# Kernel optimization log

Measured on AMD Instinct MI355X. Metric: run time of the kernel, lower is better.

The kernel has to match this reference:

```python
import jax, jax.numpy as jnp
import numpy as np

N = 50000   # nodes
E = 800000  # edges (avg degree 16)
F = 128     # node_features


def setup_inputs() -> dict:
    key = jax.random.key(0)
    ks = jax.random.split(key, 10)
    s = 1.0 / np.sqrt(F)
    x = jax.random.normal(ks[0], (N, F), jnp.float32)
    edge_index = jax.random.randint(ks[1], (2, E), 0, N, dtype=jnp.int32)
    edge_weight = jax.random.uniform(ks[2], (E,), jnp.float32)
    # EvolveGCNO initial weight (glorot-ish) and GRU parameters (PyTorch layout)
    W0 = jax.random.uniform(ks[3], (F, F), jnp.float32, -s, s)
    W_ih = jax.random.uniform(ks[4], (3 * F, F), jnp.float32, -s, s)
    W_hh = jax.random.uniform(ks[5], (3 * F, F), jnp.float32, -s, s)
    b_ih = jax.random.uniform(ks[6], (3 * F,), jnp.float32, -s, s)
    b_hh = jax.random.uniform(ks[7], (3 * F,), jnp.float32, -s, s)
    # Linear(F, 1) head
    w_lin = jax.random.uniform(ks[8], (1, F), jnp.float32, -s, s)
    b_lin = jax.random.uniform(ks[9], (1,), jnp.float32, -s, s)
    return dict(x=x, edge_index=edge_index, edge_weight=edge_weight, W0=W0,
                W_ih=W_ih, W_hh=W_hh, b_ih=b_ih, b_hh=b_hh,
                w_lin=w_lin, b_lin=b_lin)


def _gru_evolve(W0, W_ih, W_hh, b_ih, b_hh):
    # GRU(input=W0, hidden=W0): seq_len=1, batch=F, feature=F (PyTorch gate order r,z,n)
    gi = W0 @ W_ih.T + b_ih  # [F, 3F]
    gh = W0 @ W_hh.T + b_hh  # [F, 3F]
    f = W0.shape[1]
    i_r, i_z, i_n = gi[:, :f], gi[:, f:2 * f], gi[:, 2 * f:]
    h_r, h_z, h_n = gh[:, :f], gh[:, f:2 * f], gh[:, 2 * f:]
    r = jax.nn.sigmoid(i_r + h_r)
    z = jax.nn.sigmoid(i_z + h_z)
    n = jnp.tanh(i_n + r * h_n)
    return (1.0 - z) * n + z * W0  # evolved weight [F, F]


def reference(x, edge_index, edge_weight, W0, W_ih, W_hh, b_ih, b_hh, w_lin, b_lin):
    n_nodes = x.shape[0]
    W = _gru_evolve(W0, W_ih, W_hh, b_ih, b_hh)
    # gcn_norm: add self loops (weight 1), symmetric D^-1/2 A D^-1/2
    loop = jnp.arange(n_nodes, dtype=edge_index.dtype)
    src = jnp.concatenate([edge_index[0], loop])
    dst = jnp.concatenate([edge_index[1], loop])
    w = jnp.concatenate([edge_weight, jnp.ones((n_nodes,), x.dtype)])
    deg = jax.ops.segment_sum(w, dst, num_segments=n_nodes)
    dinv = jnp.where(deg > 0, jax.lax.rsqrt(deg), 0.0)
    norm = dinv[src] * w * dinv[dst]  # [E+N]
    xw = x @ W  # [N, F]
    h = jax.ops.segment_sum(norm[:, None] * xw[src], dst, num_segments=n_nodes)
    h = jnp.tanh(h)
    return h @ w_lin.T + b_lin  # [N, 1]
```

## Files before the change

### kernel.cpp

```cpp
#include <hip/hip_runtime.h>
#include <hip/hip_bf16.h>
#include <math.h>

#define N_NODES 50000
#define N_EDGES 800000
#define FDIM 128
#define SCAN_BLOCKS 196
#define XW_BLOCKS 391

typedef unsigned int uint32;
typedef __attribute__((ext_vector_type(8))) __bf16 bf16x8;
typedef __attribute__((ext_vector_type(8))) short short8;
typedef __attribute__((ext_vector_type(16))) float f32x16;

#define FLAG_A 200
#define FLAG_B 201
#define SCANNED 256

__device__ inline unsigned short f2bf(float f) {
  unsigned int u = __float_as_uint(f);
  unsigned int r = u + 0x7fffu + ((u >> 16) & 1u);
  return (unsigned short)(r >> 16);
}

__global__ __launch_bounds__(384) void evolve_kernel(
    const float* __restrict__ W0, const float* __restrict__ Wih,
    const float* __restrict__ Whh, const float* __restrict__ bih,
    const float* __restrict__ bhh, float* __restrict__ W,
    int* __restrict__ cnt, int* __restrict__ part) {
  int i = blockIdx.x;
  int jj = threadIdx.x;
  int gid = i * 384 + jj;
  for (int j = gid; j < N_NODES; j += 128 * 384) cnt[j] = 0;
  if (gid == 0) part[FLAG_A] = 0;
  if (gid == 1) part[FLAG_B] = 0;

  __shared__ float w0s[FDIM];
  __shared__ float gis[3 * FDIM];
  __shared__ float ghs[3 * FDIM];
  if (jj < FDIM) w0s[jj] = W0[i * FDIM + jj];
  __syncthreads();
  float gi = bih[jj], gh = bhh[jj];
  const float4* wih4 = (const float4*)(Wih + jj * FDIM);
  const float4* whh4 = (const float4*)(Whh + jj * FDIM);
#pragma unroll 8
  for (int k = 0; k < FDIM / 4; k++) {
    float4 a = wih4[k];
    float4 b = whh4[k];
    float w0a = w0s[4 * k], w0b = w0s[4 * k + 1];
    float w0c = w0s[4 * k + 2], w0d = w0s[4 * k + 3];
    gi += a.x * w0a + a.y * w0b + a.z * w0c + a.w * w0d;
    gh += b.x * w0a + b.y * w0b + b.z * w0c + b.w * w0d;
  }
  gis[jj] = gi;
  ghs[jj] = gh;
  __syncthreads();
  if (jj < FDIM) {
    float r = 1.0f / (1.0f + expf(-(gis[jj] + ghs[jj])));
    float z = 1.0f / (1.0f + expf(-(gis[jj + FDIM] + ghs[jj + FDIM])));
    float nn = tanhf(gis[jj + 2 * FDIM] + r * ghs[jj + 2 * FDIM]);
    W[i * FDIM + jj] = (1.0f - z) * nn + z * w0s[jj];
  }
}

__global__ __launch_bounds__(256) void histxw_kernel(
    const int* __restrict__ ei, int* __restrict__ cnt, int* __restrict__ rank,
    const float* __restrict__ x, const float* __restrict__ W,
    unsigned short* __restrict__ y, int n) {
  __shared__ short Bs[16 * 128 * 8];
  int t = threadIdx.x;
  if (blockIdx.x >= XW_BLOCKS) {
    int idx = (blockIdx.x - XW_BLOCKS) * 256 + t;
    if (idx < N_EDGES) {
      int dst = ei[N_EDGES + idx];
      rank[idx] = atomicAdd(&cnt[dst], 1);
    }
    return;
  }
#pragma unroll
  for (int i = 0; i < 64; i++) {
    int idx = i * 256 + t;
    int k = idx >> 7, nn = idx & 127;
    Bs[(((k >> 3) << 7) + nn) * 8 + (k & 7)] = (short)f2bf(W[idx]);
  }
  __syncthreads();

  int lane = t & 63;
  int wid = blockIdx.x * 4 + (t >> 6);
  int tr = wid * 32;
  if (tr >= n) return;
  int m = lane & 31;
  int q2 = lane >> 5;

  int row = tr + m;
  if (row >= n) row = n - 1;
  const float* xr = x + (size_t)row * FDIM;

  bf16x8 a[8];
#pragma unroll
  for (int kc = 0; kc < 8; kc++) {
    int k0 = kc * 16 + q2 * 8;
    float4 p = *(const float4*)(xr + k0);
    float4 q = *(const float4*)(xr + k0 + 4);
    short8 s;
    s[0] = (short)f2bf(p.x); s[1] = (short)f2bf(p.y);
    s[2] = (short)f2bf(p.z); s[3] = (short)f2bf(p.w);
    s[4] = (short)f2bf(q.x); s[5] = (short)f2bf(q.y);
    s[6] = (short)f2bf(q.z); s[7] = (short)f2bf(q.w);
    a[kc] = __builtin_bit_cast(bf16x8, s);
  }

  f32x16 acc[4];
#pragma unroll
  for (int ct = 0; ct < 4; ct++) {
#pragma unroll
    for (int r = 0; r < 16; r++) acc[ct][r] = 0.0f;
  }
#pragma unroll
  for (int ct = 0; ct < 4; ct++) {
    int nn = ct * 32 + m;
#pragma unroll
    for (int kc = 0; kc < 8; kc++) {
      int kg = kc * 2 + q2;
      bf16x8 b = __builtin_bit_cast(
          bf16x8, *(const short8*)(Bs + (((kg << 7) + nn) << 3)));
      acc[ct] = __builtin_amdgcn_mfma_f32_32x32x16_bf16(a[kc], b, acc[ct], 0,
                                                        0, 0);
    }
  }

#pragma unroll
  for (int r = 0; r < 16; r++) {
    int rl = (r & 3) + ((r >> 2) << 3) + (q2 << 2);
    int rg = tr + rl;
    if (rg < n) {
#pragma unroll
      for (int ct = 0; ct < 4; ct++) {
        y[(size_t)rg * FDIM + ct * 32 + m] = f2bf(acc[ct][r]);
      }
    }
  }
}

__global__ __launch_bounds__(256) void scan_all_kernel(
    const int* __restrict__ cnt, int* __restrict__ part, int* __restrict__ offs,
    int n) {
  __shared__ int tmp[256];
  int t = threadIdx.x;
  int bid = blockIdx.x;
  int idx = bid * 256 + t;
  int v = (idx < n) ? cnt[idx] : 0;
  tmp[t] = v;
  __syncthreads();
#pragma unroll
  for (int off = 1; off < 256; off <<= 1) {
    int u = (t >= off) ? tmp[t - off] : 0;
    __syncthreads();
    tmp[t] += u;
    __syncthreads();
  }
  int local_excl = tmp[t] - v;
  int block_sum = tmp[255];
  if (t == 0) {
    __hip_atomic_store(&part[bid], block_sum, __ATOMIC_RELEASE,
                       __HIP_MEMORY_SCOPE_AGENT);
    __hip_atomic_fetch_add(&part[FLAG_A], 1, __ATOMIC_ACQ_REL,
                           __HIP_MEMORY_SCOPE_AGENT);
  }
  if (bid == 0) {
    if (t == 0) {
      while (__hip_atomic_load(&part[FLAG_A], __ATOMIC_ACQUIRE,
                               __HIP_MEMORY_SCOPE_AGENT) < SCAN_BLOCKS) {
        __builtin_amdgcn_s_sleep(1);
      }
    }
    __syncthreads();
    __shared__ int ps[256];
    int pv = (t < SCAN_BLOCKS)
                 ? __hip_atomic_load(&part[t], __ATOMIC_RELAXED,
                                     __HIP_MEMORY_SCOPE_AGENT)
                 : 0;
    ps[t] = pv;
    __syncthreads();
#pragma unroll
    for (int off = 1; off < 256; off <<= 1) {
      int u = (t >= off) ? ps[t - off] : 0;
      __syncthreads();
      ps[t] += u;
      __syncthreads();
    }
    if (t < SCAN_BLOCKS)
      __hip_atomic_store(&part[SCANNED + t], ps[t] - pv, __ATOMIC_RELAXED,
                         __HIP_MEMORY_SCOPE_AGENT);
    __syncthreads();
    if (t == 0)
      __hip_atomic_store(&part[FLAG_B], 1, __ATOMIC_RELEASE,
                         __HIP_MEMORY_SCOPE_AGENT);
  }
  if (t == 0) {
    while (__hip_atomic_load(&part[FLAG_B], __ATOMIC_ACQUIRE,
                             __HIP_MEMORY_SCOPE_AGENT) == 0) {
      __builtin_amdgcn_s_sleep(1);
    }
  }
  __syncthreads();
  int base = __hip_atomic_load(&part[SCANNED + bid], __ATOMIC_RELAXED,
                               __HIP_MEMORY_SCOPE_AGENT);
  int excl = base + local_excl;
  if (idx < n) offs[idx] = excl;
  if (idx == n - 1) offs[n] = excl + v;
}

__global__ void scatter_kernel(const int* __restrict__ ei,
                               const float* __restrict__ ew,
                               const int* __restrict__ offs,
                               const int* __restrict__ rank,
                               int2* __restrict__ csr, int e) {
  int idx = blockIdx.x * blockDim.x + threadIdx.x;
  if (idx < e) {
    int src = ei[idx];
    int dst = ei[N_EDGES + idx];
    int pos = offs[dst] + rank[idx];
    csr[pos] = make_int2(src, __float_as_int(ew[idx]));
  }
}

__global__ __launch_bounds__(256) void deg_dinv_kernel(
    const int2* __restrict__ csr, const int* __restrict__ offs,
    float* __restrict__ dinv, int n) {
  int i = blockIdx.x * blockDim.x + threadIdx.x;
  if (i >= n) return;
  int b = offs[i], e = offs[i + 1];
  float d = 1.0f;
  for (int j = b; j < e; j++) d += __int_as_float(csr[j].y);
  dinv[i] = (d > 0.0f) ? rsqrtf(d) : 0.0f;
}

__global__ __launch_bounds__(256) void gather_kernel(
    const uint32* __restrict__ yb, const int* __restrict__ offs,
    const int2* __restrict__ csr, const float* __restrict__ dinv,
    const float* __restrict__ wl, const float* __restrict__ bl,
    float* __restrict__ out, int n) {
  int wid = (int)((blockIdx.x * (size_t)blockDim.x + threadIdx.x) >> 6);
  int lane = threadIdx.x & 63;
  if (wid >= n) return;
  float di = dinv[wid];
  uint32 uv = yb[(size_t)wid * 64 + lane];
  float ax = di * __uint_as_float(uv << 16);
  float ay = di * __uint_as_float(uv & 0xffff0000u);
  int beg = offs[wid], end = offs[wid + 1];
  int e = beg;
  for (; e + 4 <= end; e += 4) {
    int2 c0 = csr[e];
    int2 c1 = csr[e + 1];
    int2 c2 = csr[e + 2];
    int2 c3 = csr[e + 3];
    uint32 u0 = yb[(size_t)c0.x * 64 + lane];
    uint32 u1 = yb[(size_t)c1.x * 64 + lane];
    uint32 u2 = yb[(size_t)c2.x * 64 + lane];
    uint32 u3 = yb[(size_t)c3.x * 64 + lane];
    float w0 = __int_as_float(c0.y) * dinv[c0.x];
    float w1 = __int_as_float(c1.y) * dinv[c1.x];
    float w2 = __int_as_float(c2.y) * dinv[c2.x];
    float w3 = __int_as_float(c3.y) * dinv[c3.x];
    ax += w0 * __uint_as_float(u0 << 16);
    ay += w0 * __uint_as_float(u0 & 0xffff0000u);
    ax += w1 * __uint_as_float(u1 << 16);
    ay += w1 * __uint_as_float(u1 & 0xffff0000u);
    ax += w2 * __uint_as_float(u2 << 16);
    ay += w2 * __uint_as_float(u2 & 0xffff0000u);
    ax += w3 * __uint_as_float(u3 << 16);
    ay += w3 * __uint_as_float(u3 & 0xffff0000u);
  }
  for (; e < end; e++) {
    int2 c = csr[e];
    uint32 u = yb[(size_t)c.x * 64 + lane];
    float wn = __int_as_float(c.y) * dinv[c.x];
    ax += wn * __uint_as_float(u << 16);
    ay += wn * __uint_as_float(u & 0xffff0000u);
  }
  float2 wv = ((const float2*)wl)[lane];
  float p = tanhf(di * ax) * wv.x + tanhf(di * ay) * wv.y;
#pragma unroll
  for (int o = 32; o > 0; o >>= 1) p += __shfl_down(p, o, 64);
  if (lane == 0) out[wid] = p + bl[0];
}

extern "C" void kernel_launch(void* const* d_in, const int* in_sizes, int n_in,
                              void* d_out, int out_size, void* d_ws,
                              size_t ws_size, hipStream_t stream) {
  const float* x = (const float*)d_in[0];
  const int* ei = (const int*)d_in[1];
  const float* ew = (const float*)d_in[2];
  const float* W0 = (const float*)d_in[3];
  const float* Wih = (const float*)d_in[4];
  const float* Whh = (const float*)d_in[5];
  const float* bih = (const float*)d_in[6];
  const float* bhh = (const float*)d_in[7];
  const float* wl = (const float*)d_in[8];
  const float* bl = (const float*)d_in[9];
  float* out = (float*)d_out;

  float* ws = (float*)d_ws;
  float* W_ev = ws;
  unsigned short* y = (unsigned short*)(W_ev + 16384);
  float* dinv = (float*)(y + (size_t)N_NODES * FDIM);
  int* cnt = (int*)(dinv + N_NODES);
  int* rank = cnt + N_NODES;
  int* offs = rank + N_EDGES;
  int2* csr = (int2*)(offs + 50004);
  int* part = (int*)(csr + N_EDGES);

  evolve_kernel<<<FDIM, 384, 0, stream>>>(W0, Wih, Whh, bih, bhh, W_ev, cnt,
                                          part);
  histxw_kernel<<<XW_BLOCKS + (N_EDGES + 255) / 256, 256, 0, stream>>>(
      ei, cnt, rank, x, W_ev, y, N_NODES);
  scan_all_kernel<<<SCAN_BLOCKS, 256, 0, stream>>>(cnt, part, offs, N_NODES);
  scatter_kernel<<<(N_EDGES + 255) / 256, 256, 0, stream>>>(ei, ew, offs, rank,
                                                            csr, N_EDGES);
  deg_dinv_kernel<<<(N_NODES + 255) / 256, 256, 0, stream>>>(csr, offs, dinv,
                                                             N_NODES);
  gather_kernel<<<(N_NODES * 64) / 256, 256, 0, stream>>>(
      (const uint32*)y, offs, csr, dinv, wl, bl, out, N_NODES);
}
```

Baseline: 212.3 us.

## Fuse pipeline into two persistent kernels with grid barriers and prenormalized CSR weights

Merges the GRU evolve step into the histogram/XW kernel, with an atomic spin-wait gating the matmul blocks, and replaces the scan, scatter and degree kernels with one 196-block kernel that uses software grid barriers. It also precomputes the full symmetric normalization into the CSR weights, so the gather no longer loads dinv per edge, and unrolls the gather loop 8-wide. The aim is to cut launch overhead and the random dinv lookups in the gather. The risks are spin-wait stalls, or deadlock if not all blocks are co-resident, plus an extra serial pass over the CSR data.

Result: slower. 296.4 us (+39.6%).

```diff
diff --git a/kernel.cpp b/kernel.cpp
--- a/kernel.cpp
+++ b/kernel.cpp
@@ -5,17 +5,19 @@
 #define N_NODES 50000
 #define N_EDGES 800000
 #define FDIM 128
-#define SCAN_BLOCKS 196
+#define D2_BLOCKS 196
 #define XW_BLOCKS 391
+#define HIST_BLOCKS 3125
 
 typedef unsigned int uint32;
 typedef __attribute__((ext_vector_type(8))) __bf16 bf16x8;
 typedef __attribute__((ext_vector_type(8))) short short8;
 typedef __attribute__((ext_vector_type(16))) float f32x16;
 
-#define FLAG_A 200
-#define FLAG_B 201
-#define SCANNED 256
+#define EVOLVE_DONE 0
+#define BAR0 1
+#define SUMS 8
+#define SCANNED 208
 
 __device__ inline unsigned short f2bf(float f) {
   unsigned int u = __float_as_uint(f);
@@ -23,60 +25,71 @@
   return (unsigned short)(r >> 16);
 }
 
-__global__ __launch_bounds__(384) void evolve_kernel(
+__global__ __launch_bounds__(256) void mega1_kernel(
     const float* __restrict__ W0, const float* __restrict__ Wih,
     const float* __restrict__ Whh, const float* __restrict__ bih,
     const float* __restrict__ bhh, float* __restrict__ W,
-    int* __restrict__ cnt, int* __restrict__ part) {
-  int i = blockIdx.x;
-  int jj = threadIdx.x;
-  int gid = i * 384 + jj;
-  for (int j = gid; j < N_NODES; j += 128 * 384) cnt[j] = 0;
-  if (gid == 0) part[FLAG_A] = 0;
-  if (gid == 1) part[FLAG_B] = 0;
-
-  __shared__ float w0s[FDIM];
-  __shared__ float gis[3 * FDIM];
-  __shared__ float ghs[3 * FDIM];
-  if (jj < FDIM) w0s[jj] = W0[i * FDIM + jj];
-  __syncthreads();
-  float gi = bih[jj], gh = bhh[jj];
-  const float4* wih4 = (const float4*)(Wih + jj * FDIM);
-  const float4* whh4 = (const float4*)(Whh + jj * FDIM);
-#pragma unroll 8
-  for (int k = 0; k < FDIM / 4; k++) {
-    float4 a = wih4[k];
-    float4 b = whh4[k];
-    float w0a = w0s[4 * k], w0b = w0s[4 * k + 1];
-    float w0c = w0s[4 * k + 2], w0d = w0s[4 * k + 3];
-    gi += a.x * w0a + a.y * w0b + a.z * w0c + a.w * w0d;
-    gh += b.x * w0a + b.y * w0b + b.z * w0c + b.w * w0d;
-  }
-  gis[jj] = gi;
-  ghs[jj] = gh;
-  __syncthreads();
-  if (jj < FDIM) {
-    float r = 1.0f / (1.0f + expf(-(gis[jj] + ghs[jj])));
-    float z = 1.0f / (1.0f + expf(-(gis[jj + FDIM] + ghs[jj + FDIM])));
-    float nn = tanhf(gis[jj + 2 * FDIM] + r * ghs[jj + 2 * FDIM]);
-    W[i * FDIM + jj] = (1.0f - z) * nn + z * w0s[jj];
-  }
-}
-
-__global__ __launch_bounds__(256) void histxw_kernel(
     const int* __restrict__ ei, int* __restrict__ cnt, int* __restrict__ rank,
-    const float* __restrict__ x, const float* __restrict__ W,
-    unsigned short* __restrict__ y, int n) {
-  __shared__ short Bs[16 * 128 * 8];
+    const float* __restrict__ x, unsigned short* __restrict__ y,
+    int* __restrict__ sync, int n) {
+  __shared__ __align__(16) char smem[32768];
   int t = threadIdx.x;
-  if (blockIdx.x >= XW_BLOCKS) {
-    int idx = (blockIdx.x - XW_BLOCKS) * 256 + t;
+  int bid = blockIdx.x;
+
+  if (bid >= XW_BLOCKS) {
+    int idx = (bid - XW_BLOCKS) * 256 + t;
     if (idx < N_EDGES) {
       int dst = ei[N_EDGES + idx];
       rank[idx] = atomicAdd(&cnt[dst], 1);
     }
     return;
   }
+
+  if (bid < FDIM) {
+    float* w0s = (float*)smem;
+    float* gis = w0s + FDIM;
+    float* ghs = gis + 3 * FDIM;
+    if (t < FDIM) w0s[t] = W0[bid * FDIM + t];
+    __syncthreads();
+    for (int jj = t; jj < 3 * FDIM; jj += 256) {
+      float gi = bih[jj], gh = bhh[jj];
+      const float4* wih4 = (const float4*)(Wih + jj * FDIM);
+      const float4* whh4 = (const float4*)(Whh + jj * FDIM);
+#pragma unroll 8
+      for (int k = 0; k < FDIM / 4; k++) {
+        float4 a = wih4[k];
+        float4 b = whh4[k];
+        float w0a = w0s[4 * k], w0b = w0s[4 * k + 1];
+        float w0c = w0s[4 * k + 2], w0d = w0s[4 * k + 3];
+        gi += a.x * w0a + a.y * w0b + a.z * w0c + a.w * w0d;
+        gh += b.x * w0a + b.y * w0b + b.z * w0c + b.w * w0d;
+      }
+      gis[jj] = gi;
+      ghs[jj] = gh;
+    }
+    __syncthreads();
+    if (t < FDIM) {
+      float r = 1.0f / (1.0f + expf(-(gis[t] + ghs[t])));
+      float z = 1.0f / (1.0f + expf(-(gis[t + FDIM] + ghs[t + FDIM])));
+      float nn = tanhf(gis[t + 2 * FDIM] + r * ghs[t + 2 * FDIM]);
+      W[bid * FDIM + t] = (1.0f - z) * nn + z * w0s[t];
+      __threadfence();
+    }
+    __syncthreads();
+    if (t == 0)
+      __hip_atomic_fetch_add(&sync[EVOLVE_DONE], 1, __ATOMIC_ACQ_REL,
+                             __HIP_MEMORY_SCOPE_AGENT);
+  }
+
+  if (t == 0) {
+    while (__hip_atomic_load(&sync[EVOLVE_DONE], __ATOMIC_ACQUIRE,
+                             __HIP_MEMORY_SCOPE_AGENT) < FDIM) {
+      __builtin_amdgcn_s_sleep(2);
+    }
+  }
+  __syncthreads();
+
+  short* Bs = (short*)smem;
 #pragma unroll
   for (int i = 0; i < 64; i++) {
     int idx = i * 256 + t;
@@ -86,7 +99,7 @@
   __syncthreads();
 
   int lane = t & 63;
-  int wid = blockIdx.x * 4 + (t >> 6);
+  int wid = bid * 4 + (t >> 6);
   int tr = wid * 32;
   if (tr >= n) return;
   int m = lane & 31;
@@ -142,13 +155,28 @@
   }
 }
 
-__global__ __launch_bounds__(256) void scan_all_kernel(
-    const int* __restrict__ cnt, int* __restrict__ part, int* __restrict__ offs,
-    int n) {
+__device__ inline void grid_bar(int* ctr, int t) {
+  __syncthreads();
+  if (t == 0) {
+    __hip_atomic_fetch_add(ctr, 1, __ATOMIC_ACQ_REL, __HIP_MEMORY_SCOPE_AGENT);
+    while (__hip_atomic_load(ctr, __ATOMIC_ACQUIRE,
+                             __HIP_MEMORY_SCOPE_AGENT) < D2_BLOCKS) {
+      __builtin_amdgcn_s_sleep(1);
+    }
+  }
+  __syncthreads();
+}
+
+__global__ __launch_bounds__(256) void mega2_kernel(
+    const int* __restrict__ ei, const float* __restrict__ ew,
+    const int* __restrict__ cnt, const int* __restrict__ rank,
+    int* __restrict__ sync, int* __restrict__ lexcl, int* __restrict__ offs,
+    int2* csr, float* __restrict__ dinv, int n) {
   __shared__ int tmp[256];
-  int t = threadIdx.x;
-  int bid = blockIdx.x;
+  int t = threadIdx.x, bid = blockIdx.x;
+  const int STRIDE = D2_BLOCKS * 256;
   int idx = bid * 256 + t;
+
   int v = (idx < n) ? cnt[idx] : 0;
   tmp[t] = v;
   __syncthreads();
@@ -159,81 +187,52 @@
     tmp[t] += u;
     __syncthreads();
   }
-  int local_excl = tmp[t] - v;
-  int block_sum = tmp[255];
-  if (t == 0) {
-    __hip_atomic_store(&part[bid], block_sum, __ATOMIC_RELEASE,
-                       __HIP_MEMORY_SCOPE_AGENT);
-    __hip_atomic_fetch_add(&part[FLAG_A], 1, __ATOMIC_ACQ_REL,
-                           __HIP_MEMORY_SCOPE_AGENT);
-  }
+  if (idx < n) lexcl[idx] = tmp[t] - v;
+  if (t == 255) sync[SUMS + bid] = tmp[255];
+  grid_bar(&sync[BAR0 + 0], t);
+
   if (bid == 0) {
-    if (t == 0) {
-      while (__hip_atomic_load(&part[FLAG_A], __ATOMIC_ACQUIRE,
-                               __HIP_MEMORY_SCOPE_AGENT) < SCAN_BLOCKS) {
-        __builtin_amdgcn_s_sleep(1);
-      }
-    }
-    __syncthreads();
-    __shared__ int ps[256];
-    int pv = (t < SCAN_BLOCKS)
-                 ? __hip_atomic_load(&part[t], __ATOMIC_RELAXED,
-                                     __HIP_MEMORY_SCOPE_AGENT)
-                 : 0;
-    ps[t] = pv;
+    int pv = (t < D2_BLOCKS) ? sync[SUMS + t] : 0;
+    tmp[t] = pv;
     __syncthreads();
 #pragma unroll
     for (int off = 1; off < 256; off <<= 1) {
-      int u = (t >= off) ? ps[t - off] : 0;
+      int u = (t >= off) ? tmp[t - off] : 0;
       __syncthreads();
-      ps[t] += u;
+      tmp[t] += u;
       __syncthreads();
     }
-    if (t < SCAN_BLOCKS)
-      __hip_atomic_store(&part[SCANNED + t], ps[t] - pv, __ATOMIC_RELAXED,
-                         __HIP_MEMORY_SCOPE_AGENT);
-    __syncthreads();
-    if (t == 0)
-      __hip_atomic_store(&part[FLAG_B], 1, __ATOMIC_RELEASE,
-                         __HIP_MEMORY_SCOPE_AGENT);
-  }
-  if (t == 0) {
-    while (__hip_atomic_load(&part[FLAG_B], __ATOMIC_ACQUIRE,
-                             __HIP_MEMORY_SCOPE_AGENT) == 0) {
-      __builtin_amdgcn_s_sleep(1);
-    }
-  }
-  __syncthreads();
-  int base = __hip_atomic_load(&part[SCANNED + bid], __ATOMIC_RELAXED,
-                               __HIP_MEMORY_SCOPE_AGENT);
-  int excl = base + local_excl;
-  if (idx < n) offs[idx] = excl;
-  if (idx == n - 1) offs[n] = excl + v;
-}
-
-__global__ void scatter_kernel(const int* __restrict__ ei,
-                               const float* __restrict__ ew,
-                               const int* __restrict__ offs,
-                               const int* __restrict__ rank,
-                               int2* __restrict__ csr, int e) {
-  int idx = blockIdx.x * blockDim.x + threadIdx.x;
-  if (idx < e) {
-    int src = ei[idx];
-    int dst = ei[N_EDGES + idx];
-    int pos = offs[dst] + rank[idx];
-    csr[pos] = make_int2(src, __float_as_int(ew[idx]));
-  }
-}
-
-__global__ __launch_bounds__(256) void deg_dinv_kernel(
-    const int2* __restrict__ csr, const int* __restrict__ offs,
-    float* __restrict__ dinv, int n) {
-  int i = blockIdx.x * blockDim.x + threadIdx.x;
-  if (i >= n) return;
-  int b = offs[i], e = offs[i + 1];
-  float d = 1.0f;
-  for (int j = b; j < e; j++) d += __int_as_float(csr[j].y);
-  dinv[i] = (d > 0.0f) ? rsqrtf(d) : 0.0f;
+    if (t < D2_BLOCKS) sync[SCANNED + t] = tmp[t] - pv;
+    if (t == D2_BLOCKS - 1) offs[n] = tmp[t];
+  }
+  grid_bar(&sync[BAR0 + 1], t);
+
+  for (int i = idx; i < n; i += STRIDE)
+    offs[i] = sync[SCANNED + (i >> 8)] + lexcl[i];
+  for (int j = idx; j < N_EDGES; j += STRIDE) {
+    int src = ei[j];
+    int dst = ei[N_EDGES + j];
+    int pos = sync[SCANNED + (dst >> 8)] + lexcl[dst] + rank[j];
+    csr[pos] = make_int2(src, __float_as_int(ew[j]));
+  }
+  grid_bar(&sync[BAR0 + 2], t);
+
+  for (int i = idx; i < n; i += STRIDE) {
+    int b = offs[i], e = offs[i + 1];
+    float d = 1.0f;
+    for (int j = b; j < e; j++) d += __int_as_float(csr[j].y);
+    dinv[i] = (d > 0.0f) ? rsqrtf(d) : 0.0f;
+  }
+  grid_bar(&sync[BAR0 + 3], t);
+
+  for (int i = idx; i < n; i += STRIDE) {
+    float dd = dinv[i];
+    int b = offs[i], e = offs[i + 1];
+    for (int j = b; j < e; j++) {
+      int2 c = csr[j];
+      csr[j].y = __float_as_int(__int_as_float(c.y) * dinv[c.x] * dd);
+    }
+  }
 }
 
 __global__ __launch_bounds__(256) void gather_kernel(
@@ -245,42 +244,35 @@
   int lane = threadIdx.x & 63;
   if (wid >= n) return;
   float di = dinv[wid];
+  float sn = di * di;
   uint32 uv = yb[(size_t)wid * 64 + lane];
-  float ax = di * __uint_as_float(uv << 16);
-  float ay = di * __uint_as_float(uv & 0xffff0000u);
+  float ax = sn * __uint_as_float(uv << 16);
+  float ay = sn * __uint_as_float(uv & 0xffff0000u);
   int beg = offs[wid], end = offs[wid + 1];
   int e = beg;
-  for (; e + 4 <= end; e += 4) {
-    int2 c0 = csr[e];
-    int2 c1 = csr[e + 1];
-    int2 c2 = csr[e + 2];
-    int2 c3 = csr[e + 3];
-    uint32 u0 = yb[(size_t)c0.x * 64 + lane];
-    uint32 u1 = yb[(size_t)c1.x * 64 + lane];
-    uint32 u2 = yb[(size_t)c2.x * 64 + lane];
-    uint32 u3 = yb[(size_t)c3.x * 64 + lane];
-    float w0 = __int_as_float(c0.y) * dinv[c0.x];
-    float w1 = __int_as_float(c1.y) * dinv[c1.x];
-    float w2 = __int_as_float(c2.y) * dinv[c2.x];
-    float w3 = __int_as_float(c3.y) * dinv[c3.x];
-    ax += w0 * __uint_as_float(u0 << 16);
-    ay += w0 * __uint_as_float(u0 & 0xffff0000u);
-    ax += w1 * __uint_as_float(u1 << 16);
-    ay += w1 * __uint_as_float(u1 & 0xffff0000u);
-    ax += w2 * __uint_as_float(u2 << 16);
-    ay += w2 * __uint_as_float(u2 & 0xffff0000u);
-    ax += w3 * __uint_as_float(u3 << 16);
-    ay += w3 * __uint_as_float(u3 & 0xffff0000u);
+  for (; e + 8 <= end; e += 8) {
+    int2 c[8];
+    uint32 u[8];
+#pragma unroll
+    for (int q = 0; q < 8; q++) c[q] = csr[e + q];
+#pragma unroll
+    for (int q = 0; q < 8; q++) u[q] = yb[(size_t)c[q].x * 64 + lane];
+#pragma unroll
+    for (int q = 0; q < 8; q++) {
+      float wn = __int_as_float(c[q].y);
+      ax += wn * __uint_as_float(u[q] << 16);
+      ay += wn * __uint_as_float(u[q] & 0xffff0000u);
+    }
   }
   for (; e < end; e++) {
     int2 c = csr[e];
     uint32 u = yb[(size_t)c.x * 64 + lane];
-    float wn = __int_as_float(c.y) * dinv[c.x];
+    float wn = __int_as_float(c.y);
     ax += wn * __uint_as_float(u << 16);
     ay += wn * __uint_as_float(u & 0xffff0000u);
   }
   float2 wv = ((const float2*)wl)[lane];
-  float p = tanhf(di * ax) * wv.x + tanhf(di * ay) * wv.y;
+  float p = tanhf(ax) * wv.x + tanhf(ay) * wv.y;
 #pragma unroll
   for (int o = 32; o > 0; o >>= 1) p += __shfl_down(p, o, 64);
   if (lane == 0) out[wid] = p + bl[0];
@@ -306,20 +298,17 @@
   unsigned short* y = (unsigned short*)(W_ev + 16384);
   float* dinv = (float*)(y + (size_t)N_NODES * FDIM);
   int* cnt = (int*)(dinv + N_NODES);
-  int* rank = cnt + N_NODES;
-  int* offs = rank + N_EDGES;
-  int2* csr = (int2*)(offs + 50004);
-  int* part = (int*)(csr + N_EDGES);
-
-  evolve_kernel<<<FDIM, 384, 0, stream>>>(W0, Wih, Whh, bih, bhh, W_ev, cnt,
-                                          part);
-  histxw_kernel<<<XW_BLOCKS + (N_EDGES + 255) / 256, 256, 0, stream>>>(
-      ei, cnt, rank, x, W_ev, y, N_NODES);
-  scan_all_kernel<<<SCAN_BLOCKS, 256, 0, stream>>>(cnt, part, offs, N_NODES);
-  scatter_kernel<<<(N_EDGES + 255) / 256, 256, 0, stream>>>(ei, ew, offs, rank,
-                                                            csr, N_EDGES);
-  deg_dinv_kernel<<<(N_NODES + 255) / 256, 256, 0, stream>>>(csr, offs, dinv,
-                                                             N_NODES);
+  int* sync = cnt + N_NODES;
+  int* rank = sync + 512;
+  int* lexcl = rank + N_EDGES;
+  int* offs = lexcl + N_NODES;
+  int2* csr = (int2*)(offs + 50008);
+
+  hipMemsetAsync(cnt, 0, sizeof(int) * (N_NODES + 512), stream);
+  mega1_kernel<<<XW_BLOCKS + HIST_BLOCKS, 256, 0, stream>>>(
+      W0, Wih, Whh, bih, bhh, W_ev, ei, cnt, rank, x, y, sync, N_NODES);
+  mega2_kernel<<<D2_BLOCKS, 256, 0, stream>>>(ei, ew, cnt, rank, sync, lexcl,
+                                              offs, csr, dinv, N_NODES);
   gather_kernel<<<(N_NODES * 64) / 256, 256, 0, stream>>>(
       (const uint32*)y, offs, csr, dinv, wl, bl, out, N_NODES);
 }
```
